# Kernel tuning notes

Measured on AMD Instinct MI355X. Metric: run time of the kernel, lower is better.

Reference implementation:

```python
import jax, jax.numpy as jnp
import numpy as np

N = 100000   # nodes
E = 1600000  # edges (avg degree 16)
IN, H, OUT, P = 100, 256, 256, 128
EPS = 1e-5


def setup_inputs() -> dict:
    key = jax.random.key(0)
    ks = jax.random.split(key, 12)

    def lin(k, o, i):
        return jax.random.normal(k, (o, i), jnp.float32) / np.float32(np.sqrt(i))

    return {
        "x": jax.random.normal(ks[0], (N, IN), jnp.float32),
        "edge_index": jax.random.randint(ks[1], (2, E), 0, N),
        # SAGEConv l (aggregated-neighbor branch, has bias) and r (root branch, no bias)
        "Wl0": lin(ks[2], H, IN), "bl0": jnp.zeros((H,), jnp.float32), "Wr0": lin(ks[3], H, IN),
        "Wl1": lin(ks[4], H, H),  "bl1": jnp.zeros((H,), jnp.float32), "Wr1": lin(ks[5], H, H),
        "Wl2": lin(ks[6], OUT, H), "bl2": jnp.zeros((OUT,), jnp.float32), "Wr2": lin(ks[7], OUT, H),
        # projection head + BatchNorm1d(128)
        "Wp": lin(ks[8], P, OUT), "bp": jnp.zeros((P,), jnp.float32),
        "gamma": jnp.ones((P,), jnp.float32), "beta": jnp.zeros((P,), jnp.float32),
    }


def _sage_conv(x, src, dst, Wl, bl, Wr):
    # PyG SAGEConv default: mean-aggregate source features into destinations,
    # then lin_l(agg) + lin_r(x).
    agg = jax.ops.segment_sum(x[src], dst, num_segments=N)           # [N, d]
    deg = jax.ops.segment_sum(jnp.ones((src.shape[0],), x.dtype), dst, num_segments=N)
    agg = agg / jnp.maximum(deg, 1.0)[:, None]
    return agg @ Wl.T + bl + x @ Wr.T


def reference(x, edge_index, Wl0, bl0, Wr0, Wl1, bl1, Wr1, Wl2, bl2, Wr2, Wp, bp, gamma, beta):
    src, dst = edge_index[0], edge_index[1]
    x = jax.nn.relu(_sage_conv(x, src, dst, Wl0, bl0, Wr0))  # dropout is identity in eval
    x = jax.nn.relu(_sage_conv(x, src, dst, Wl1, bl1, Wr1))
    x = _sage_conv(x, src, dst, Wl2, bl2, Wr2)               # no relu on last layer
    z = x @ Wp.T + bp                                        # projection head -> [N, 128]
    mu = jnp.mean(z, axis=0)
    var = jnp.var(z, axis=0)                                 # biased, as torch BN uses for normalization
    h = gamma * (z - mu) * jax.lax.rsqrt(var + EPS) + beta
    return (x, h)
```

## Files before the change

kernel.cpp:

```cpp
#include <hip/hip_runtime.h>
#include <hip/hip_bf16.h>

#define EPS_BN 1e-5f

using short8  = __attribute__((ext_vector_type(8))) short;
using ushort8 = __attribute__((ext_vector_type(8))) unsigned short;
using f32x4   = __attribute__((ext_vector_type(4))) float;

typedef const __attribute__((address_space(1))) void* gas_ptr;
typedef __attribute__((address_space(3))) void* las_ptr;

__device__ inline float bf2f(unsigned short u) {
    union { unsigned i; float f; } c; c.i = ((unsigned)u) << 16; return c.f;
}
__device__ inline unsigned short f2bf(float f) {
    unsigned x = __float_as_uint(f);
    unsigned r = (x + 0x7FFF + ((x >> 16) & 1)) >> 16;
    return (unsigned short)r;
}

__global__ void zero_i32(int* __restrict__ p, int n) {
    int i = blockIdx.x * blockDim.x + threadIdx.x;
    if (i < n) p[i] = 0;
}
__global__ void zero_f32(float* __restrict__ p, int n) {
    int i = blockIdx.x * blockDim.x + threadIdx.x;
    if (i < n) p[i] = 0.0f;
}

__global__ void zero_rows(unsigned short* __restrict__ xpad,
                          unsigned short* __restrict__ h1,
                          unsigned short* __restrict__ h2, int n) {
    int t = threadIdx.x;
    if (t < 128) xpad[(size_t)n * 128 + t] = 0;
    h1[(size_t)n * 256 + t] = 0;
    h2[(size_t)n * 256 + t] = 0;
}

__global__ void conv_w(const float* __restrict__ w, unsigned short* __restrict__ o,
                       int R, int C, int CP) {
    int t = blockIdx.x * blockDim.x + threadIdx.x;
    if (t >= R * CP) return;
    int r = t / CP, c = t % CP;
    o[t] = (c < C) ? f2bf(w[(size_t)r * C + c]) : (unsigned short)0;
}

__global__ void conv_x_pad(const float* __restrict__ x, unsigned short* __restrict__ xp, int n) {
    int t = blockIdx.x * blockDim.x + threadIdx.x;
    if (t >= n * 32) return;
    int node = t >> 5, g = t & 31;
    int f0 = g * 4;
    ushort4 o;
    const float* xr = x + (size_t)node * 100;
    o.x = (f0 + 0 < 100) ? f2bf(xr[f0 + 0]) : 0;
    o.y = (f0 + 1 < 100) ? f2bf(xr[f0 + 1]) : 0;
    o.z = (f0 + 2 < 100) ? f2bf(xr[f0 + 2]) : 0;
    o.w = (f0 + 3 < 100) ? f2bf(xr[f0 + 3]) : 0;
    *(ushort4*)(xp + (size_t)node * 128 + f0) = o;
}

__global__ void count_k(const int* __restrict__ dst, int* __restrict__ counts, int E) {
    int i = blockIdx.x * blockDim.x + threadIdx.x;
    if (i < E) atomicAdd(&counts[dst[i]], 1);
}

__global__ void scan1(const int* __restrict__ counts, int* __restrict__ rp,
                      int* __restrict__ partials, int n) {
    __shared__ int s[256];
    int t = threadIdx.x;
    int i = blockIdx.x * 256 + t;
    int v = (i < n) ? ((counts[i] + 7) & ~7) : 0;
    s[t] = v;
    __syncthreads();
    for (int off = 1; off < 256; off <<= 1) {
        int u = (t >= off) ? s[t - off] : 0;
        __syncthreads();
        s[t] += u;
        __syncthreads();
    }
    if (i < n) rp[i] = s[t] - v;
    if (t == 255) partials[blockIdx.x] = s[255];
}

__global__ void scan2(int* __restrict__ partials, int nb) {
    __shared__ int s[512];
    int t = threadIdx.x;
    int v = (t < nb) ? partials[t] : 0;
    s[t] = v;
    __syncthreads();
    for (int off = 1; off < 512; off <<= 1) {
        int u = (t >= off) ? s[t - off] : 0;
        __syncthreads();
        s[t] += u;
        __syncthreads();
    }
    if (t < nb) partials[t] = s[t] - v;
}

__global__ void scan3(int* __restrict__ rp, const int* __restrict__ partials, int n) {
    int i = blockIdx.x * blockDim.x + threadIdx.x;
    if (i < n) rp[i] += partials[i >> 8];
}

__global__ void fill_k(const int* __restrict__ src, const int* __restrict__ dst,
                       const int* __restrict__ rp, int* __restrict__ cursor,
                       int* __restrict__ col, int E) {
    int i = blockIdx.x * blockDim.x + threadIdx.x;
    if (i < E) {
        int d = dst[i];
        int pos = atomicAdd(&cursor[d], 1);
        col[rp[d] + pos] = src[i];
    }
}

__global__ void pad_fill(const int* __restrict__ rp, const int* __restrict__ cnt,
                         int* __restrict__ col, int n, int zrow) {
    int node = blockIdx.x * blockDim.x + threadIdx.x;
    if (node >= n) return;
    int d = cnt[node];
    int s = rp[node] + d;
    int e = rp[node] + ((d + 7) & ~7);
    for (int i = s; i < e; ++i) col[i] = zrow;
}

__global__ __launch_bounds__(256) void agg_bf16_256(
    const unsigned short* __restrict__ x, const int* __restrict__ rp,
    const int* __restrict__ cnt, const int* __restrict__ col,
    unsigned short* __restrict__ out, int n) {
    int wave = threadIdx.x >> 6, lane = threadIdx.x & 63;
    int node = blockIdx.x * 4 + wave;
    if (node >= n) return;
    int s = rp[node];
    int deg = cnt[node];
    int nb8 = (deg + 7) >> 3;
    int h = lane >> 5;
    int l32 = lane & 31;
    const size_t coff = (size_t)l32 * 8;

    float a[8] = {0, 0, 0, 0, 0, 0, 0, 0};
    int i = s + h;
    int b = 0;
    for (; b + 2 <= nb8; b += 2, i += 16) {
        int r0 = col[i],     r1 = col[i + 2],  r2 = col[i + 4],  r3 = col[i + 6];
        int r4 = col[i + 8], r5 = col[i + 10], r6 = col[i + 12], r7 = col[i + 14];
        ushort8 v0 = *(const ushort8*)(x + (size_t)r0 * 256 + coff);
        ushort8 v1 = *(const ushort8*)(x + (size_t)r1 * 256 + coff);
        ushort8 v2 = *(const ushort8*)(x + (size_t)r2 * 256 + coff);
        ushort8 v3 = *(const ushort8*)(x + (size_t)r3 * 256 + coff);
        ushort8 v4 = *(const ushort8*)(x + (size_t)r4 * 256 + coff);
        ushort8 v5 = *(const ushort8*)(x + (size_t)r5 * 256 + coff);
        ushort8 v6 = *(const ushort8*)(x + (size_t)r6 * 256 + coff);
        ushort8 v7 = *(const ushort8*)(x + (size_t)r7 * 256 + coff);
#pragma unroll
        for (int j = 0; j < 8; ++j)
            a[j] += ((bf2f(v0[j]) + bf2f(v1[j])) + (bf2f(v2[j]) + bf2f(v3[j]))) +
                    ((bf2f(v4[j]) + bf2f(v5[j])) + (bf2f(v6[j]) + bf2f(v7[j])));
    }
    if (b < nb8) {
        int r0 = col[i], r1 = col[i + 2], r2 = col[i + 4], r3 = col[i + 6];
        ushort8 v0 = *(const ushort8*)(x + (size_t)r0 * 256 + coff);
        ushort8 v1 = *(const ushort8*)(x + (size_t)r1 * 256 + coff);
        ushort8 v2 = *(const ushort8*)(x + (size_t)r2 * 256 + coff);
        ushort8 v3 = *(const ushort8*)(x + (size_t)r3 * 256 + coff);
#pragma unroll
        for (int j = 0; j < 8; ++j)
            a[j] += (bf2f(v0[j]) + bf2f(v1[j])) + (bf2f(v2[j]) + bf2f(v3[j]));
    }
#pragma unroll
    for (int j = 0; j < 8; ++j) a[j] += __shfl_xor(a[j], 32);

    if (h == 0) {
        float sc = 1.0f / fmaxf((float)deg, 1.0f);
        ushort8 o;
#pragma unroll
        for (int j = 0; j < 8; ++j) o[j] = f2bf(a[j] * sc);
        *(ushort8*)(out + (size_t)node * 256 + l32 * 8) = o;
    }
}

__global__ __launch_bounds__(256) void agg_bf16_128(
    const unsigned short* __restrict__ x, const int* __restrict__ rp,
    const int* __restrict__ cnt, const int* __restrict__ col,
    unsigned short* __restrict__ out, int n) {
    int wave = threadIdx.x >> 6, lane = threadIdx.x & 63;
    int node = blockIdx.x * 4 + wave;
    if (node >= n) return;
    int s = rp[node];
    int deg = cnt[node];
    int nb8 = (deg + 7) >> 3;
    int q = lane >> 4;
    int l16 = lane & 15;
    const size_t coff = (size_t)l16 * 8;

    float a[8] = {0, 0, 0, 0, 0, 0, 0, 0};
    int i = s + q;
    int b = 0;
    for (; b + 2 <= nb8; b += 2, i += 16) {
        int r0 = col[i], r1 = col[i + 4], r2 = col[i + 8], r3 = col[i + 12];
        ushort8 v0 = *(const ushort8*)(x + (size_t)r0 * 128 + coff);
        ushort8 v1 = *(const ushort8*)(x + (size_t)r1 * 128 + coff);
        ushort8 v2 = *(const ushort8*)(x + (size_t)r2 * 128 + coff);
        ushort8 v3 = *(const ushort8*)(x + (size_t)r3 * 128 + coff);
#pragma unroll
        for (int j = 0; j < 8; ++j)
            a[j] += (bf2f(v0[j]) + bf2f(v1[j])) + (bf2f(v2[j]) + bf2f(v3[j]));
    }
    if (b < nb8) {
        int r0 = col[i], r1 = col[i + 4];
        ushort8 v0 = *(const ushort8*)(x + (size_t)r0 * 128 + coff);
        ushort8 v1 = *(const ushort8*)(x + (size_t)r1 * 128 + coff);
#pragma unroll
        for (int j = 0; j < 8; ++j) a[j] += bf2f(v0[j]) + bf2f(v1[j]);
    }
#pragma unroll
    for (int j = 0; j < 8; ++j) {
        a[j] += __shfl_xor(a[j], 16);
        a[j] += __shfl_xor(a[j], 32);
    }

    if (lane < 16) {
        float sc = 1.0f / fmaxf((float)deg, 1.0f);
        ushort8 o;
#pragma unroll
        for (int j = 0; j < 8; ++j) o[j] = f2bf(a[j] * sc);
        *(ushort8*)(out + (size_t)node * 128 + l16 * 8) = o;
    }
}

template <int KTOT, int DOUT, bool HAS_AGG, bool RELU, bool STF32, bool STBF16>
__global__ __launch_bounds__(512) void sage_mfma(
    const unsigned short* __restrict__ xp, const unsigned short* __restrict__ ap,
    const unsigned short* __restrict__ Wr, const unsigned short* __restrict__ Wl,
    const float* __restrict__ bias,
    float* __restrict__ outf, unsigned short* __restrict__ outb, int n) {
    constexpr int CT = DOUT / 16;
    constexpr int CTW = DOUT / 64;
    constexpr int NSRC = HAS_AGG ? 2 : 1;
    constexpr int CHUNKS = NSRC * CT;
    constexpr int CPW = CHUNKS / 8;
    constexpr int KS = KTOT / 32;
    constexpr int BUFSZ = CHUNKS * 512;
    __shared__ __align__(16) unsigned short lds[2 * BUFSZ];

    const int t = threadIdx.x;
    const int wave = t >> 6, lane = t & 63;
    const int wm = wave >> 2, wn = wave & 3;
    const int lcol = lane & 15, lq = lane >> 4;
    const int node0 = blockIdx.x * 128 + wm * 64;

    auto stage = [&](int ks, int buf) {
        unsigned short* base = lds + buf * BUFSZ;
#pragma unroll
        for (int i = 0; i < CPW; ++i) {
            int chunk = wave * CPW + i;
            int srcSel = chunk / CT, ct = chunk % CT;
            const unsigned short* W = (srcSel == 0) ? Wr : Wl;
            const unsigned short* g = W + (size_t)(ct * 16 + lcol) * KTOT + ks * 32 + lq * 8;
            unsigned short* l = base + chunk * 512;
            __builtin_amdgcn_global_load_lds((gas_ptr)g, (las_ptr)l, 16, 0, 0);
        }
    };

    const unsigned short* aPx[4];
    const unsigned short* aPa[4];
#pragma unroll
    for (int mt = 0; mt < 4; ++mt) {
        aPx[mt] = xp + (size_t)(node0 + mt * 16 + lcol) * KTOT + lq * 8;
        if (HAS_AGG) aPa[mt] = ap + (size_t)(node0 + mt * 16 + lcol) * KTOT + lq * 8;
    }
    auto LOADA = [&](int ks, short8 (&ax)[4], short8 (&aa)[4]) {
#pragma unroll
        for (int mt = 0; mt < 4; ++mt) {
            ax[mt] = *(const short8*)(aPx[mt] + ks * 32);
            if (HAS_AGG) aa[mt] = *(const short8*)(aPa[mt] + ks * 32);
        }
    };

    f32x4 acc[4][CTW];
#pragma unroll
    for (int ct = 0; ct < CTW; ++ct) {
        float b = bias[wn * CTW * 16 + ct * 16 + lcol];
#pragma unroll
        for (int mt = 0; mt < 4; ++mt) {
            acc[mt][ct][0] = b; acc[mt][ct][1] = b; acc[mt][ct][2] = b; acc[mt][ct][3] = b;
        }
    }

    auto COMPUTE = [&](int buf, short8 (&ax)[4], short8 (&aa)[4]) {
        const unsigned short* base = lds + buf * BUFSZ;
        short8 br[CTW], bl[CTW];
#pragma unroll
        for (int c = 0; c < CTW; ++c) {
            br[c] = *(const short8*)(base + (wn * CTW + c) * 512 + lane * 8);
            if (HAS_AGG) bl[c] = *(const short8*)(base + (CT + wn * CTW + c) * 512 + lane * 8);
        }
#pragma unroll
        for (int mt = 0; mt < 4; ++mt)
#pragma unroll
            for (int c = 0; c < CTW; ++c) {
                acc[mt][c] = __builtin_amdgcn_mfma_f32_16x16x32_bf16(
                    ax[mt], br[c], acc[mt][c], 0, 0, 0);
                if (HAS_AGG)
                    acc[mt][c] = __builtin_amdgcn_mfma_f32_16x16x32_bf16(
                        aa[mt], bl[c], acc[mt][c], 0, 0, 0);
            }
    };

    short8 axE[4], aaE[4], axO[4], aaO[4];

    stage(0, 0);
    LOADA(0, axE, aaE);
    __syncthreads();

#pragma unroll
    for (int ks = 0; ks < KS; ks += 2) {
        if (ks + 1 < KS) { stage(ks + 1, 1); LOADA(ks + 1, axO, aaO); }
        COMPUTE(0, axE, aaE);
        __syncthreads();
        if (ks + 2 < KS) { stage(ks + 2, 0); LOADA(ks + 2, axE, aaE); }
        if (ks + 1 < KS) {
            COMPUTE(1, axO, aaO);
            __syncthreads();
        }
    }

#pragma unroll
    for (int mt = 0; mt < 4; ++mt) {
        int row0 = node0 + mt * 16 + lq * 4;
        if (row0 >= n) continue;
#pragma unroll
        for (int ct = 0; ct < CTW; ++ct) {
            f32x4 v = acc[mt][ct];
            if (RELU) {
                v[0] = fmaxf(v[0], 0.0f); v[1] = fmaxf(v[1], 0.0f);
                v[2] = fmaxf(v[2], 0.0f); v[3] = fmaxf(v[3], 0.0f);
            }
            int colI = wn * CTW * 16 + ct * 16 + lcol;
#pragma unroll
            for (int j = 0; j < 4; ++j) {
                int row = row0 + j;
                if (row < n) {
                    if (STF32) outf[(size_t)row * DOUT + colI] = v[j];
                    if (STBF16) outb[(size_t)row * DOUT + colI] = f2bf(v[j]);
                }
            }
        }
    }
}

__global__ void bn_partial(const float* __restrict__ z, float* __restrict__ sums, int n) {
    int f = threadIdx.x & 127;
    int half = threadIdx.x >> 7;
    float s = 0.0f, s2 = 0.0f;
    for (int row = blockIdx.x * 2 + half; row < n; row += gridDim.x * 2) {
        float v = z[(size_t)row * 128 + f];
        s += v; s2 += v * v;
    }
    __shared__ float ls[256], ls2[256];
    ls[threadIdx.x] = s; ls2[threadIdx.x] = s2;
    __syncthreads();
    if (half == 0) {
        atomicAdd(&sums[f], s + ls[128 + f]);
        atomicAdd(&sums[128 + f], s2 + ls2[128 + f]);
    }
}

__global__ void bn_finalize(const float* __restrict__ sums, const float* __restrict__ gamma,
                            const float* __restrict__ beta, float* __restrict__ params, int n) {
    int f = threadIdx.x;
    float mu = sums[f] / (float)n;
    float var = sums[128 + f] / (float)n - mu * mu;
    float inv = rsqrtf(var + EPS_BN);
    float sc = gamma[f] * inv;
    params[f] = sc;
    params[128 + f] = beta[f] - mu * sc;
}

__global__ void bn_apply(float* __restrict__ z, const float* __restrict__ params, int total4) {
    int i = blockIdx.x * blockDim.x + threadIdx.x;
    for (; i < total4; i += gridDim.x * blockDim.x) {
        float4 v = ((float4*)z)[i];
        int f0 = (i & 31) * 4;
        v.x = v.x * params[f0 + 0] + params[128 + f0 + 0];
        v.y = v.y * params[f0 + 1] + params[128 + f0 + 1];
        v.z = v.z * params[f0 + 2] + params[128 + f0 + 2];
        v.w = v.w * params[f0 + 3] + params[128 + f0 + 3];
        ((float4*)z)[i] = v;
    }
}

extern "C" void kernel_launch(void* const* d_in, const int* in_sizes, int n_in,
                              void* d_out, int out_size, void* d_ws, size_t ws_size,
                              hipStream_t stream) {
    const float* x_in  = (const float*)d_in[0];
    const int*   ei    = (const int*)d_in[1];
    const float* Wl0   = (const float*)d_in[2];
    const float* bl0   = (const float*)d_in[3];
    const float* Wr0   = (const float*)d_in[4];
    const float* Wl1   = (const float*)d_in[5];
    const float* bl1   = (const float*)d_in[6];
    const float* Wr1   = (const float*)d_in[7];
    const float* Wl2   = (const float*)d_in[8];
    const float* bl2   = (const float*)d_in[9];
    const float* Wr2   = (const float*)d_in[10];
    const float* Wp    = (const float*)d_in[11];
    const float* bp    = (const float*)d_in[12];
    const float* gamma = (const float*)d_in[13];
    const float* beta  = (const float*)d_in[14];

    const int IN = 100, INP = 128, H = 256, OUT = 256, P = 128;
    const int n = in_sizes[0] / IN;
    const int E = in_sizes[1] / 2;
    const int* src = ei;
    const int* dst = ei + E;

    size_t off = 0;
    auto alloc = [&](size_t bytes) -> char* {
        char* p = (char*)d_ws + off;
        off += (bytes + 255) & ~(size_t)255;
        return p;
    };
    int*   counts   = (int*)alloc((size_t)n * 4);
    int*   cursor   = (int*)alloc((size_t)n * 4);
    int*   rp       = (int*)alloc((size_t)(n + 1) * 4);
    int*   partials = (int*)alloc(512 * 4);
    int*   col      = (int*)alloc(((size_t)E + 8 * (size_t)n) * 4);
    unsigned short* Wl0b = (unsigned short*)alloc((size_t)H * INP * 2);
    unsigned short* Wr0b = (unsigned short*)alloc((size_t)H * INP * 2);
    unsigned short* Wl1b = (unsigned short*)alloc((size_t)H * H * 2);
    unsigned short* Wr1b = (unsigned short*)alloc((size_t)H * H * 2);
    unsigned short* Wl2b = (unsigned short*)alloc((size_t)OUT * H * 2);
    unsigned short* Wr2b = (unsigned short*)alloc((size_t)OUT * H * 2);
    unsigned short* Wpb  = (unsigned short*)alloc((size_t)P * OUT * 2);
    float* bnsums   = (float*)alloc(256 * 4);
    float* bnparams = (float*)alloc(256 * 4);
    unsigned short* xpad   = (unsigned short*)alloc((size_t)(n + 1) * INP * 2);
    unsigned short* aggpad = (unsigned short*)alloc((size_t)n * INP * 2);
    unsigned short* h1b    = (unsigned short*)alloc((size_t)(n + 1) * H * 2);
    unsigned short* agg1   = (unsigned short*)alloc((size_t)n * H * 2);
    unsigned short* h2b    = (unsigned short*)alloc((size_t)(n + 1) * H * 2);
    (void)alloc((size_t)256 * 512);

    unsigned short* agg2 = h1b;
    unsigned short* xb2  = xpad;

    float* out_x = (float*)d_out;
    float* z     = out_x + (size_t)n * OUT;

    const int nb = (n + 255) / 256;

    zero_i32<<<nb, 256, 0, stream>>>(counts, n);
    zero_i32<<<nb, 256, 0, stream>>>(cursor, n);
    zero_f32<<<1, 256, 0, stream>>>(bnsums, 256);
    count_k<<<(E + 255) / 256, 256, 0, stream>>>(dst, counts, E);
    scan1<<<nb, 256, 0, stream>>>(counts, rp, partials, n);
    scan2<<<1, 512, 0, stream>>>(partials, nb);
    scan3<<<nb, 256, 0, stream>>>(rp, partials, n);
    fill_k<<<(E + 255) / 256, 256, 0, stream>>>(src, dst, rp, cursor, col, E);
    pad_fill<<<nb, 256, 0, stream>>>(rp, counts, col, n, n);

    conv_x_pad<<<(n * 32 + 255) / 256, 256, 0, stream>>>(x_in, xpad, n);
    zero_rows<<<1, 256, 0, stream>>>(xpad, h1b, h2b, n);
    conv_w<<<(H * INP + 255) / 256, 256, 0, stream>>>(Wl0, Wl0b, H, IN, INP);
    conv_w<<<(H * INP + 255) / 256, 256, 0, stream>>>(Wr0, Wr0b, H, IN, INP);
    conv_w<<<(H * H + 255) / 256, 256, 0, stream>>>(Wl1, Wl1b, H, H, H);
    conv_w<<<(H * H + 255) / 256, 256, 0, stream>>>(Wr1, Wr1b, H, H, H);
    conv_w<<<(OUT * H + 255) / 256, 256, 0, stream>>>(Wl2, Wl2b, OUT, H, H);
    conv_w<<<(OUT * H + 255) / 256, 256, 0, stream>>>(Wr2, Wr2b, OUT, H, H);
    conv_w<<<(P * OUT + 255) / 256, 256, 0, stream>>>(Wp, Wpb, P, OUT, OUT);

    const int gemm_grid = (n + 127) / 128;

    agg_bf16_128<<<(n + 3) / 4, 256, 0, stream>>>(xpad, rp, counts, col, aggpad, n);
    sage_mfma<128, 256, true, true, false, true><<<gemm_grid, 512, 0, stream>>>(
        xpad, aggpad, Wr0b, Wl0b, bl0, nullptr, h1b, n);

    agg_bf16_256<<<(n + 3) / 4, 256, 0, stream>>>(h1b, rp, counts, col, agg1, n);
    sage_mfma<256, 256, true, true, false, true><<<gemm_grid, 512, 0, stream>>>(
        h1b, agg1, Wr1b, Wl1b, bl1, nullptr, h2b, n);

    agg_bf16_256<<<(n + 3) / 4, 256, 0, stream>>>(h2b, rp, counts, col, agg2, n);
    sage_mfma<256, 256, true, false, true, true><<<gemm_grid, 512, 0, stream>>>(
        h2b, agg2, Wr2b, Wl2b, bl2, out_x, xb2, n);

    sage_mfma<256, 128, false, false, true, false><<<gemm_grid, 512, 0, stream>>>(
        xb2, nullptr, Wpb, nullptr, bp, z, nullptr, n);

    bn_partial<<<256, 256, 0, stream>>>(z, bnsums, n);
    bn_finalize<<<1, 128, 0, stream>>>(bnsums, gamma, beta, bnparams, n);
    bn_apply<<<2048, 256, 0, stream>>>(z, bnparams, n * (P / 4));
}
```

Baseline: 873.0 us.

## Split GEMM output columns across grid y, drop double-buffering, read fp32 projection input

```diff
diff --git a/kernel.cpp b/kernel.cpp
--- a/kernel.cpp
+++ b/kernel.cpp
@@ -227,101 +227,94 @@
     }
 }
 
-template <int KTOT, int DOUT, bool HAS_AGG, bool RELU, bool STF32, bool STBF16>
-__global__ __launch_bounds__(512) void sage_mfma(
-    const unsigned short* __restrict__ xp, const unsigned short* __restrict__ ap,
+template <int KTOT, int DOUT, bool HAS_AGG, bool A_F32, bool RELU, bool STF32, bool STBF16>
+__global__ __launch_bounds__(256) void sage_mfma(
+    const void* __restrict__ xpv, const unsigned short* __restrict__ ap,
     const unsigned short* __restrict__ Wr, const unsigned short* __restrict__ Wl,
     const float* __restrict__ bias,
     float* __restrict__ outf, unsigned short* __restrict__ outb, int n) {
-    constexpr int CT = DOUT / 16;
-    constexpr int CTW = DOUT / 64;
     constexpr int NSRC = HAS_AGG ? 2 : 1;
-    constexpr int CHUNKS = NSRC * CT;
-    constexpr int CPW = CHUNKS / 8;
+    constexpr int CHUNKS = NSRC * 8;
+    constexpr int CPW = CHUNKS / 4;
     constexpr int KS = KTOT / 32;
-    constexpr int BUFSZ = CHUNKS * 512;
-    __shared__ __align__(16) unsigned short lds[2 * BUFSZ];
+    __shared__ __align__(16) unsigned short lds[CHUNKS * 512];
 
     const int t = threadIdx.x;
     const int wave = t >> 6, lane = t & 63;
-    const int wm = wave >> 2, wn = wave & 3;
+    const int wm = wave >> 1, wn = wave & 1;
     const int lcol = lane & 15, lq = lane >> 4;
     const int node0 = blockIdx.x * 128 + wm * 64;
-
-    auto stage = [&](int ks, int buf) {
-        unsigned short* base = lds + buf * BUFSZ;
+    const int col_base = blockIdx.y * 128;
+    const int col0 = col_base + wn * 64;
+
+    f32x4 acc[4][4];
+#pragma unroll
+    for (int c = 0; c < 4; ++c) {
+        float b = bias[col0 + c * 16 + lcol];
+#pragma unroll
+        for (int mt = 0; mt < 4; ++mt) {
+            acc[mt][c][0] = b; acc[mt][c][1] = b; acc[mt][c][2] = b; acc[mt][c][3] = b;
+        }
+    }
+
+    const unsigned short* aPx[4];
+    const float* aPxF[4];
+    const unsigned short* aPa[4];
+#pragma unroll
+    for (int mt = 0; mt < 4; ++mt) {
+        size_t row = (size_t)(node0 + mt * 16 + lcol);
+        if constexpr (A_F32) aPxF[mt] = (const float*)xpv + row * KTOT + lq * 8;
+        else                 aPx[mt]  = (const unsigned short*)xpv + row * KTOT + lq * 8;
+        if constexpr (HAS_AGG) aPa[mt] = ap + row * KTOT + lq * 8;
+    }
+
+    for (int ks = 0; ks < KS; ++ks) {
+        short8 ax[4], aa[4];
+#pragma unroll
+        for (int mt = 0; mt < 4; ++mt) {
+            if constexpr (A_F32) {
+                float4 f0 = *(const float4*)(aPxF[mt] + ks * 32);
+                float4 f1 = *(const float4*)(aPxF[mt] + ks * 32 + 4);
+                ax[mt][0] = (short)f2bf(f0.x); ax[mt][1] = (short)f2bf(f0.y);
+                ax[mt][2] = (short)f2bf(f0.z); ax[mt][3] = (short)f2bf(f0.w);
+                ax[mt][4] = (short)f2bf(f1.x); ax[mt][5] = (short)f2bf(f1.y);
+                ax[mt][6] = (short)f2bf(f1.z); ax[mt][7] = (short)f2bf(f1.w);
+            } else {
+                ax[mt] = *(const short8*)(aPx[mt] + ks * 32);
+            }
+            if constexpr (HAS_AGG) aa[mt] = *(const short8*)(aPa[mt] + ks * 32);
+        }
 #pragma unroll
         for (int i = 0; i < CPW; ++i) {
             int chunk = wave * CPW + i;
-            int srcSel = chunk / CT, ct = chunk % CT;
+            int srcSel = chunk >> 3, ct = chunk & 7;
             const unsigned short* W = (srcSel == 0) ? Wr : Wl;
-            const unsigned short* g = W + (size_t)(ct * 16 + lcol) * KTOT + ks * 32 + lq * 8;
-            unsigned short* l = base + chunk * 512;
-            __builtin_amdgcn_global_load_lds((gas_ptr)g, (las_ptr)l, 16, 0, 0);
+            const unsigned short* g =
+                W + (size_t)(col_base + ct * 16 + lcol) * KTOT + ks * 32 + lq * 8;
+            __builtin_amdgcn_global_load_lds((gas_ptr)g, (las_ptr)(lds + chunk * 512),
+                                             16, 0, 0);
         }
-    };
-
-    const unsigned short* aPx[4];
-    const unsigned short* aPa[4];
-#pragma unroll
-    for (int mt = 0; mt < 4; ++mt) {
-        aPx[mt] = xp + (size_t)(node0 + mt * 16 + lcol) * KTOT + lq * 8;
-        if (HAS_AGG) aPa[mt] = ap + (size_t)(node0 + mt * 16 + lcol) * KTOT + lq * 8;
-    }
-    auto LOADA = [&](int ks, short8 (&ax)[4], short8 (&aa)[4]) {
-#pragma unroll
-        for (int mt = 0; mt < 4; ++mt) {
-            ax[mt] = *(const short8*)(aPx[mt] + ks * 32);
-            if (HAS_AGG) aa[mt] = *(const short8*)(aPa[mt] + ks * 32);
+        __syncthreads();
+
+#pragma unroll
+        for (int s = 0; s < NSRC; ++s) {
+            short8 bf[4];
+#pragma unroll
+            for (int c = 0; c < 4; ++c)
+                bf[c] = *(const short8*)(lds + (s * 8 + wn * 4 + c) * 512 + lane * 8);
+#pragma unroll
+            for (int mt = 0; mt < 4; ++mt)
+#pragma unroll
+                for (int c = 0; c < 4; ++c) {
+                    if (s == 0)
+                        acc[mt][c] = __builtin_amdgcn_mfma_f32_16x16x32_bf16(
+                            ax[mt], bf[c], acc[mt][c], 0, 0, 0);
+                    else
+                        acc[mt][c] = __builtin_amdgcn_mfma_f32_16x16x32_bf16(
+                            aa[mt], bf[c], acc[mt][c], 0, 0, 0);
+                }
         }
-    };
-
-    f32x4 acc[4][CTW];
-#pragma unroll
-    for (int ct = 0; ct < CTW; ++ct) {
-        float b = bias[wn * CTW * 16 + ct * 16 + lcol];
-#pragma unroll
-        for (int mt = 0; mt < 4; ++mt) {
-            acc[mt][ct][0] = b; acc[mt][ct][1] = b; acc[mt][ct][2] = b; acc[mt][ct][3] = b;
-        }
-    }
-
-    auto COMPUTE = [&](int buf, short8 (&ax)[4], short8 (&aa)[4]) {
-        const unsigned short* base = lds + buf * BUFSZ;
-        short8 br[CTW], bl[CTW];
-#pragma unroll
-        for (int c = 0; c < CTW; ++c) {
-            br[c] = *(const short8*)(base + (wn * CTW + c) * 512 + lane * 8);
-            if (HAS_AGG) bl[c] = *(const short8*)(base + (CT + wn * CTW + c) * 512 + lane * 8);
-        }
-#pragma unroll
-        for (int mt = 0; mt < 4; ++mt)
-#pragma unroll
-            for (int c = 0; c < CTW; ++c) {
-                acc[mt][c] = __builtin_amdgcn_mfma_f32_16x16x32_bf16(
-                    ax[mt], br[c], acc[mt][c], 0, 0, 0);
-                if (HAS_AGG)
-                    acc[mt][c] = __builtin_amdgcn_mfma_f32_16x16x32_bf16(
-                        aa[mt], bl[c], acc[mt][c], 0, 0, 0);
-            }
-    };
-
-    short8 axE[4], aaE[4], axO[4], aaO[4];
-
-    stage(0, 0);
-    LOADA(0, axE, aaE);
-    __syncthreads();
-
-#pragma unroll
-    for (int ks = 0; ks < KS; ks += 2) {
-        if (ks + 1 < KS) { stage(ks + 1, 1); LOADA(ks + 1, axO, aaO); }
-        COMPUTE(0, axE, aaE);
-        __syncthreads();
-        if (ks + 2 < KS) { stage(ks + 2, 0); LOADA(ks + 2, axE, aaE); }
-        if (ks + 1 < KS) {
-            COMPUTE(1, axO, aaO);
-            __syncthreads();
-        }
+        __syncthreads();
     }
 
 #pragma unroll
@@ -329,20 +322,18 @@
         int row0 = node0 + mt * 16 + lq * 4;
         if (row0 >= n) continue;
 #pragma unroll
-        for (int ct = 0; ct < CTW; ++ct) {
-            f32x4 v = acc[mt][ct];
+        for (int c = 0; c < 4; ++c) {
+            f32x4 v = acc[mt][c];
             if (RELU) {
                 v[0] = fmaxf(v[0], 0.0f); v[1] = fmaxf(v[1], 0.0f);
                 v[2] = fmaxf(v[2], 0.0f); v[3] = fmaxf(v[3], 0.0f);
             }
-            int colI = wn * CTW * 16 + ct * 16 + lcol;
+            int colI = col0 + c * 16 + lcol;
 #pragma unroll
             for (int j = 0; j < 4; ++j) {
-                int row = row0 + j;
-                if (row < n) {
-                    if (STF32) outf[(size_t)row * DOUT + colI] = v[j];
-                    if (STBF16) outb[(size_t)row * DOUT + colI] = f2bf(v[j]);
-                }
+                size_t row = (size_t)row0 + j;
+                if (STF32) outf[row * DOUT + colI] = v[j];
+                if (STBF16) outb[row * DOUT + colI] = f2bf(v[j]);
             }
         }
     }
@@ -442,7 +433,6 @@
     (void)alloc((size_t)256 * 512);
 
     unsigned short* agg2 = h1b;
-    unsigned short* xb2  = xpad;
 
     float* out_x = (float*)d_out;
     float* z     = out_x + (size_t)n * OUT;
@@ -469,22 +459,22 @@
     conv_w<<<(OUT * H + 255) / 256, 256, 0, stream>>>(Wr2, Wr2b, OUT, H, H);
     conv_w<<<(P * OUT + 255) / 256, 256, 0, stream>>>(Wp, Wpb, P, OUT, OUT);
 
-    const int gemm_grid = (n + 127) / 128;
+    const int gx = (n + 127) / 128;
 
     agg_bf16_128<<<(n + 3) / 4, 256, 0, stream>>>(xpad, rp, counts, col, aggpad, n);
-    sage_mfma<128, 256, true, true, false, true><<<gemm_grid, 512, 0, stream>>>(
+    sage_mfma<128, 256, true, false, true, false, true><<<dim3(gx, 2), 256, 0, stream>>>(
         xpad, aggpad, Wr0b, Wl0b, bl0, nullptr, h1b, n);
 
     agg_bf16_256<<<(n + 3) / 4, 256, 0, stream>>>(h1b, rp, counts, col, agg1, n);
-    sage_mfma<256, 256, true, true, false, true><<<gemm_grid, 512, 0, stream>>>(
+    sage_mfma<256, 256, true, false, true, false, true><<<dim3(gx, 2), 256, 0, stream>>>(
         h1b, agg1, Wr1b, Wl1b, bl1, nullptr, h2b, n);
 
     agg_bf16_256<<<(n + 3) / 4, 256, 0, stream>>>(h2b, rp, counts, col, agg2, n);
-    sage_mfma<256, 256, true, false, true, true><<<gemm_grid, 512, 0, stream>>>(
-        h2b, agg2, Wr2b, Wl2b, bl2, out_x, xb2, n);
-
-    sage_mfma<256, 128, false, false, true, false><<<gemm_grid, 512, 0, stream>>>(
-        xb2, nullptr, Wpb, nullptr, bp, z, nullptr, n);
+    sage_mfma<256, 256, true, false, false, true, false><<<dim3(gx, 2), 256, 0, stream>>>(
+        h2b, agg2, Wr2b, Wl2b, bl2, out_x, nullptr, n);
+
+    sage_mfma<256, 128, false, true, false, true, false><<<dim3(gx, 1), 256, 0, stream>>>(
+        out_x, nullptr, Wpb, nullptr, bp, z, nullptr, n);
 
     bn_partial<<<256, 256, 0, stream>>>(z, bnsums, n);
     bn_finalize<<<1, 128, 0, stream>>>(bnsums, gamma, beta, bnparams, n);
```

After: 837.3 us. 4.1% less time.
